# Optimization experiments

Hardware: AMD Instinct MI355X
Metric: run time of the kernel (lower is better)

The kernel has to match this reference:

```python
import jax, jax.numpy as jnp
import numpy as np
import math

DN = ('NCHW', 'OIHW', 'NCHW')

def conv2d(x, w, b=None, pad=0):
    y = jax.lax.conv_general_dilated(x, w, (1, 1), [(pad, pad), (pad, pad)], dimension_numbers=DN)
    if b is not None:
        y = y + b[None, :, None, None]
    return y

def group_norm(x, weight, bias, groups=32, eps=1e-5):
    B, C, H, W = x.shape
    xg = x.reshape(B, groups, C // groups, H, W)
    mean = xg.mean(axis=(2, 3, 4), keepdims=True)
    var = xg.var(axis=(2, 3, 4), keepdims=True)
    xg = (xg - mean) * jax.lax.rsqrt(var + eps)
    return xg.reshape(B, C, H, W) * weight[None, :, None, None] + bias[None, :, None, None]

def swish(x):
    return x * jax.nn.sigmoid(x)

def setup_inputs() -> dict:
    key = jax.random.key(0)
    ks = jax.random.split(key, 20)
    B, C, H, W = 8, 192, 48, 48
    emb = 192
    n_div = 12
    Cq = C // n_div  # 16
    s = 0.02
    return {
        'x': jax.random.normal(ks[0], (B, C, H, W), jnp.float32),
        'xe': jax.random.normal(ks[1], (B, C, H, W), jnp.float32),
        'time_emb': jax.random.normal(ks[2], (B, emb), jnp.float32),
        'gn1_w': jnp.ones((C,), jnp.float32),
        'gn1_b': jnp.zeros((C,), jnp.float32),
        'conv1_w': jax.random.normal(ks[3], (C, C, 3, 3), jnp.float32) * s,
        'conv1_b': jnp.zeros((C,), jnp.float32),
        'aff_w': jax.random.normal(ks[4], (2 * C, emb), jnp.float32) * s,
        'aff_b': jnp.zeros((2 * C,), jnp.float32),
        'gn2_w': jnp.ones((C,), jnp.float32),
        'gn2_b': jnp.zeros((C,), jnp.float32),
        'conv2_w': jax.random.normal(ks[5], (C, C, 3, 3), jnp.float32) * s,
        'conv2_b': jnp.zeros((C,), jnp.float32),
        'q_w': jax.random.normal(ks[6], (Cq, C, 1, 1), jnp.float32) * s,
        'kv_w': jax.random.normal(ks[7], (2 * Cq, C, 1, 1), jnp.float32) * s,
        'out_w': jax.random.normal(ks[8], (C, Cq, 3, 3), jnp.float32) * s,
        'out_b': jnp.zeros((C,), jnp.float32),
    }

def reference(x, xe, time_emb, gn1_w, gn1_b, conv1_w, conv1_b, aff_w, aff_b,
              gn2_w, gn2_b, conv2_w, conv2_b, q_w, kv_w, out_w, out_b):
    B, C, H, W = x.shape
    n_head, n_div = 1, 12
    head_dim = C // (n_head * n_div)

    # ----- ResnetBlock -----
    h = conv2d(swish(group_norm(x, gn1_w, gn1_b)), conv1_w, conv1_b, pad=1)
    # FeatureWiseAffine (use_affine_level=True)
    gb = time_emb @ aff_w.T + aff_b          # [B, 2C]
    gamma, beta = jnp.split(gb, 2, axis=1)   # each [B, C]
    gb_sum = 0.5 * (gamma + beta)[:, :, None, None]
    h = h + gb_sum * h + gb_sum
    h = conv2d(swish(group_norm(h, gn2_w, gn2_b)), conv2_w, conv2_b, pad=1)
    xres = h + x  # res_conv is Identity (dim == dim_out)

    # ----- CrossAttention -----
    Ye, Xe = xe.shape[-2], xe.shape[-1]
    query = conv2d(xres, q_w).reshape(B, n_head, head_dim, H, W)
    kv = conv2d(xe, kv_w).reshape(B, n_head, head_dim * 2, Ye, Xe)
    key_, value = jnp.split(kv, 2, axis=2)
    scale = 1.0 / math.sqrt(C // n_div)
    attn = jnp.einsum('bnchw,bncyx->bnhwyx', query, key_) * scale
    attn = jax.nn.softmax(attn.reshape(B, n_head, H, W, -1), axis=-1)
    attn = attn.reshape(B, n_head, H, W, Ye, Xe)
    out = jnp.einsum('bnhwyx,bncyx->bnchw', attn, value)
    out = conv2d(out.reshape(B, C // n_div, H, W), out_w, out_b, pad=1)
    return out + xres
```

## Files before the change

kernel.cpp:

```cpp
#include <hip/hip_runtime.h>
#include <hip/hip_bf16.h>

#define NB 8
#define NC 192
#define NH 48
#define NW 48
#define NP 2304
#define NGROUPS 32
#define CPG 6
#define NEMB 192
#define NCQ 16

#define PH 50
#define PWS 52
#define ACT_T_ELEMS ((size_t)NB * PH * PWS * NC)
#define AOT_ELEMS   ((size_t)NB * PH * PWS * 16)

typedef __attribute__((ext_vector_type(4))) short s16x4;
typedef __attribute__((ext_vector_type(8))) short s16x8;
typedef __attribute__((ext_vector_type(4))) float f32x4;

static __device__ inline short f2bf(float v) {
  __hip_bfloat16 h = __float2bfloat16(v);
  return *(short*)&h;
}

__global__ __launch_bounds__(256) void megaprep_kernel(
    const float* __restrict__ conv1w, const float* __restrict__ conv2w,
    const float* __restrict__ outw, const float* __restrict__ qw,
    const float* __restrict__ kvw, const float* __restrict__ emb,
    const float* __restrict__ affw, const float* __restrict__ affb,
    short* __restrict__ wbuf1, short* __restrict__ wbuf2, short* __restrict__ wbufo,
    short* __restrict__ awq, short* __restrict__ awkv,
    float* __restrict__ gbsum, short* __restrict__ actt, short* __restrict__ aot) {
  int bx = blockIdx.x;
  int tid = threadIdx.x;
  const float SC = 0.36067376022224085f;
  if (bx < 2592) {
    const float* w = (bx < 1296) ? conv1w : conv2w;
    short* wb      = (bx < 1296) ? wbuf1 : wbuf2;
    int i = ((bx < 1296) ? bx : bx - 1296) * 256 + tid;
    int j  = i & 7;
    int l  = (i >> 3) & 63;
    int cf = (i >> 9) % 12;
    int tk = (i >> 9) / 12;
    int t  = tk % 9;
    int kc = tk / 9;
    int co = cf * 16 + (l & 15);
    int ci = kc * 32 + (l >> 4) * 8 + j;
    wb[i] = f2bf(w[((size_t)co * NC + ci) * 9 + t]);
  } else if (bx < 2808) {
    int i = (bx - 2592) * 256 + tid;
    int j  = i & 7;
    int l  = (i >> 3) & 63;
    int cf = (i >> 9) % 12;
    int t  = (i >> 9) / 12;
    int co = cf * 16 + (l & 15);
    int ci = (l >> 4) * 8 + j;
    wbufo[i] = (ci < 16) ? f2bf(outw[((size_t)co * 16 + ci) * 9 + t]) : (short)0;
  } else if (bx < 2820) {
    int i = (bx - 2808) * 256 + tid;
    int j = i & 7, l = (i >> 3) & 63, rest = i >> 9;
    int kc = rest;
    int co = (l & 15);
    int ci = kc * 32 + (l >> 4) * 8 + j;
    awq[i] = f2bf(qw[(size_t)co * NC + ci] * SC);
  } else if (bx < 2844) {
    int i = (bx - 2820) * 256 + tid;
    int j = i & 7, l = (i >> 3) & 63, rest = i >> 9;
    int m = rest % 2, kc = rest / 2;
    int co = m * 16 + (l & 15);
    int ci = kc * 32 + (l >> 4) * 8 + j;
    awkv[i] = f2bf(kvw[(size_t)co * NC + ci]);
  } else if (bx < 2850) {
    int i = (bx - 2844) * 256 + tid;
    if (i < NB * NC) {
      int b = i / NC;
      int c = i - b * NC;
      const float* e  = emb + b * NEMB;
      const float* w0 = affw + c * NEMB;
      const float* w1 = affw + (c + NC) * NEMB;
      float s = 0.f;
      for (int j = 0; j < NEMB; ++j) s += e[j] * (w0[j] + w1[j]);
      gbsum[i] = 0.5f * (s + affb[c] + affb[c + NC]);
    }
  } else if (bx < 3154) {
    int rel = bx - 2850;
    int b = rel / 38, xb = rel - b * 38;
    int i = xb * 256 + tid;
    if (i < 9600) {
      int c4 = i % 48;
      int r  = i / 48;
      size_t off;
      if (r < 52)       off = ((size_t)0 * PWS + r) * NC;
      else if (r < 104) off = ((size_t)49 * PWS + (r - 52)) * NC;
      else if (r < 152) off = ((size_t)(r - 104 + 1) * PWS + 0) * NC;
      else              off = ((size_t)(r - 152 + 1) * PWS + 49) * NC;
      *(s16x4*)(&actt[(size_t)b * PH * PWS * NC + off + c4 * 4]) = (s16x4){0, 0, 0, 0};
    }
  } else {
    int b = bx - 3154;
    for (int i = tid; i < 784; i += 256) {
      int c4  = i & 3;
      int pos = i >> 2;
      int r, col;
      if (pos < 50)       { r = 0;  col = pos; }
      else if (pos < 100) { r = 49; col = pos - 50; }
      else if (pos < 148) { r = pos - 100 + 1; col = 0; }
      else                { r = pos - 148 + 1; col = 49; }
      *(s16x4*)(&aot[(((size_t)b * PH + r) * PWS + col) * 16 + c4 * 4]) = (s16x4){0, 0, 0, 0};
    }
  }
}

__global__ __launch_bounds__(192) void gn_stats_part_kernel(const float* __restrict__ in,
                                                            float* __restrict__ part) {
  int bg = blockIdx.x, seg = blockIdx.y;
  const float4* p = (const float4*)(in + (size_t)bg * (CPG * NP) + seg * 2304);
  float s = 0.f, s2 = 0.f;
  for (int i = threadIdx.x; i < 576; i += 192) {
    float4 v = p[i];
    s  += v.x + v.y + v.z + v.w;
    s2 += v.x * v.x + v.y * v.y + v.z * v.z + v.w * v.w;
  }
#pragma unroll
  for (int off = 32; off > 0; off >>= 1) {
    s  += __shfl_down(s, off);
    s2 += __shfl_down(s2, off);
  }
  __shared__ float red[6];
  int wave = threadIdx.x >> 6;
  if ((threadIdx.x & 63) == 0) { red[wave * 2] = s; red[wave * 2 + 1] = s2; }
  __syncthreads();
  if (threadIdx.x == 0) {
    part[(bg * 6 + seg) * 2]     = red[0] + red[2] + red[4];
    part[(bg * 6 + seg) * 2 + 1] = red[1] + red[3] + red[5];
  }
}

__global__ __launch_bounds__(256) void gn_apply_t_kernel(const float* __restrict__ in,
                                                         const float* __restrict__ gnpart,
                                                         const float* __restrict__ gw,
                                                         const float* __restrict__ gb,
                                                         short* __restrict__ actt) {
  __shared__ float tile[48 * 193];
  __shared__ float sst[32][2];
  int bh = blockIdx.x;
  int b = bh / NH;
  int h = bh - b * NH;
  int tid = threadIdx.x;
  if (tid < 32) {
    float S = 0.f, S2 = 0.f;
#pragma unroll
    for (int k = 0; k < 6; ++k) {
      S  += gnpart[((b * 32 + tid) * 6 + k) * 2];
      S2 += gnpart[((b * 32 + tid) * 6 + k) * 2 + 1];
    }
    const float invN = 1.f / (float)(CPG * NP);
    float mean = S * invN;
    float var  = S2 * invN - mean * mean;
    sst[tid][0] = mean;
    sst[tid][1] = rsqrtf(var + 1e-5f);
  }
  __syncthreads();
  for (int i = tid; i < 2304; i += 256) {
    int c = i / 12;
    int w = (i % 12) * 4;
    float4 v = *(const float4*)(in + (((size_t)b * NC + c) * NH + h) * NW + w);
    float sc = sst[c / CPG][1] * gw[c];
    float sh = gb[c] - sst[c / CPG][0] * sc;
    float y;
    y = v.x * sc + sh; tile[(w + 0) * 193 + c] = y / (1.f + __expf(-y));
    y = v.y * sc + sh; tile[(w + 1) * 193 + c] = y / (1.f + __expf(-y));
    y = v.z * sc + sh; tile[(w + 2) * 193 + c] = y / (1.f + __expf(-y));
    y = v.w * sc + sh; tile[(w + 3) * 193 + c] = y / (1.f + __expf(-y));
  }
  __syncthreads();
  short* dst = actt + (((size_t)b * PH + h + 1) * PWS + 1) * NC;
  for (int i = tid; i < 2304; i += 256) {
    int w  = i / 48;
    int c4 = (i - w * 48) * 4;
    s16x4 o;
    o.x = f2bf(tile[w * 193 + c4 + 0]);
    o.y = f2bf(tile[w * 193 + c4 + 1]);
    o.z = f2bf(tile[w * 193 + c4 + 2]);
    o.w = f2bf(tile[w * 193 + c4 + 3]);
    *(s16x4*)(dst + (size_t)w * NC + c4) = o;
  }
}

template <int NM, bool ISKV>
__global__ __launch_bounds__(192) void qkv_fused_kernel(const float* __restrict__ X,
                                                        const short* __restrict__ aw,
                                                        short* __restrict__ KQ,
                                                        short* __restrict__ VTb) {
  __shared__ float tile[48 * 193];
  int bh = blockIdx.x;
  int b = bh / NH;
  int h = bh - b * NH;
  int tid = threadIdx.x;
  for (int i = tid; i < 2304; i += 192) {
    int c = i / 12;
    int w = (i % 12) * 4;
    float4 v = *(const float4*)(X + (((size_t)b * NC + c) * NH + h) * NW + w);
    tile[(w + 0) * 193 + c] = v.x;
    tile[(w + 1) * 193 + c] = v.y;
    tile[(w + 2) * 193 + c] = v.z;
    tile[(w + 3) * 193 + c] = v.w;
  }
  __syncthreads();
  int lane = tid & 63, wv = tid >> 6;
  int g = lane >> 4, ql = lane & 15;
  int pxl = wv * 16 + ql;
  int p   = h * NW + pxl;

  f32x4 acc[NM];
#pragma unroll
  for (int m = 0; m < NM; ++m) acc[m] = (f32x4){0.f, 0.f, 0.f, 0.f};

  const float* bp = &tile[pxl * 193 + g * 8];
#pragma unroll
  for (int kc = 0; kc < 6; ++kc) {
    s16x8 bf;
#pragma unroll
    for (int j = 0; j < 8; ++j) bf[j] = f2bf(bp[kc * 32 + j]);
#pragma unroll
    for (int m = 0; m < NM; ++m) {
      s16x8 af = *(const s16x8*)(aw + ((size_t)(kc * NM + m) * 64 + lane) * 8);
      acc[m] = __builtin_amdgcn_mfma_f32_16x16x32_bf16(af, bf, acc[m], 0, 0, 0);
    }
  }
  s16x4 o0;
  o0.x = f2bf(acc[0][0]); o0.y = f2bf(acc[0][1]);
  o0.z = f2bf(acc[0][2]); o0.w = f2bf(acc[0][3]);
  *(s16x4*)(KQ + ((size_t)b * NP + p) * 32 + g * 4) = o0;
  *(s16x4*)(KQ + ((size_t)b * NP + p) * 32 + 16 + g * 4) = (s16x4){0, 0, 0, 0};
  if (ISKV) {
#pragma unroll
    for (int r = 0; r < 4; ++r)
      VTb[((size_t)b * 16 + g * 4 + r) * NP + p] = f2bf(acc[NM - 1][r]);
  }
}

template <bool AFFINE, bool RESID>
__global__ __launch_bounds__(256) void conv_mfma_kernel(const short* __restrict__ actt,
                                                        const short* __restrict__ wbuf,
                                                        const float* __restrict__ bias,
                                                        const float* __restrict__ gbsum,
                                                        const float* __restrict__ resid,
                                                        float* __restrict__ out) {
  __shared__ short S[2][4][50][40];
  int bs = blockIdx.x;
  int b = bs / 24;
  int strip = bs - b * 24;
  int coB = blockIdx.y;
  int h0 = strip * 2;
  int tid = threadIdx.x;
  int lane = tid & 63, wave = tid >> 6;
  int wy = wave >> 1, wx = wave & 1;
  int g8 = (lane >> 4) * 8;

  f32x4 acc[2][3];
#pragma unroll
  for (int m = 0; m < 2; ++m)
#pragma unroll
    for (int f = 0; f < 3; ++f) acc[m][f] = (f32x4){0.f, 0.f, 0.f, 0.f};

  const size_t actbase = ((size_t)b * PH + h0) * PWS * NC;

  auto stage = [&](int buf, int kc) {
    for (int i = tid; i < 800; i += 256) {
      int ci8 = i & 3;
      int rc  = i >> 2;
      int col = rc % 50, r = rc / 50;
      const s16x8* src = (const s16x8*)(actt + actbase + ((size_t)r * PWS + col) * NC +
                                        kc * 32 + ci8 * 8);
      *(s16x8*)(&S[buf][r][col][ci8 * 8]) = *src;
    }
  };

  stage(0, 0);
  __syncthreads();
  for (int kc = 0; kc < 6; ++kc) {
    if (kc < 5) stage((kc + 1) & 1, kc + 1);
    int cur = kc & 1;
#pragma unroll
    for (int t = 0; t < 9; ++t) {
      int ky = t / 3, kx = t - ky * 3;
      const short* wp = wbuf + ((((size_t)kc * 9 + t) * 12 + (coB * 4 + wy * 2)) * 64 + lane) * 8;
      s16x8 a0 = *(const s16x8*)wp;
      s16x8 a1 = *(const s16x8*)(wp + 64 * 8);
      int row = wx + ky;
#pragma unroll
      for (int f = 0; f < 3; ++f) {
        int col = f * 16 + (lane & 15) + kx;
        s16x8 bf = *(const s16x8*)(&S[cur][row][col][g8]);
        acc[0][f] = __builtin_amdgcn_mfma_f32_16x16x32_bf16(a0, bf, acc[0][f], 0, 0, 0);
        acc[1][f] = __builtin_amdgcn_mfma_f32_16x16x32_bf16(a1, bf, acc[1][f], 0, 0, 0);
      }
    }
    __syncthreads();
  }
  int hout = h0 + wx;
#pragma unroll
  for (int m = 0; m < 2; ++m) {
    int co0 = coB * 64 + wy * 32 + m * 16;
#pragma unroll
    for (int r = 0; r < 4; ++r) {
      int co = co0 + (lane >> 4) * 4 + r;
      float bv = bias[co];
      float s = AFFINE ? gbsum[b * NC + co] : 0.f;
#pragma unroll
      for (int f = 0; f < 3; ++f) {
        int w = f * 16 + (lane & 15);
        size_t o = (((size_t)b * NC + co) * NH + hout) * NW + w;
        float v = acc[m][f][r] + bv;
        if (AFFINE) v = v * (1.f + s) + s;
        if (RESID) v += resid[o];
        out[o] = v;
      }
    }
  }
}

__global__ __launch_bounds__(256) void out_conv_mfma_kernel(const short* __restrict__ aot,
                                                            const short* __restrict__ wbuf,
                                                            const float* __restrict__ bias,
                                                            float* __restrict__ out) {
  __shared__ short S[4][50][40];
  int bs = blockIdx.x;
  int b = bs / 24;
  int strip = bs - b * 24;
  int coB = blockIdx.y;
  int h0 = strip * 2;
  int tid = threadIdx.x;
  int lane = tid & 63, wave = tid >> 6;
  int wy = wave >> 1, wx = wave & 1;
  int g8 = (lane >> 4) * 8;

  f32x4 acc[2][3];
#pragma unroll
  for (int m = 0; m < 2; ++m)
#pragma unroll
    for (int f = 0; f < 3; ++f) acc[m][f] = (f32x4){0.f, 0.f, 0.f, 0.f};

  const size_t base = ((size_t)b * PH + h0) * PWS * 16;
  for (int i = tid; i < 800; i += 256) {
    int ci8 = i & 3;
    int rc  = i >> 2;
    int col = rc % 50, r = rc / 50;
    s16x8 v = (s16x8){0, 0, 0, 0, 0, 0, 0, 0};
    if (ci8 < 2)
      v = *(const s16x8*)(aot + base + ((size_t)r * PWS + col) * 16 + ci8 * 8);
    *(s16x8*)(&S[r][col][ci8 * 8]) = v;
  }
  __syncthreads();
#pragma unroll
  for (int t = 0; t < 9; ++t) {
    int ky = t / 3, kx = t - ky * 3;
    const short* wp = wbuf + (((size_t)t * 12 + (coB * 4 + wy * 2)) * 64 + lane) * 8;
    s16x8 a0 = *(const s16x8*)wp;
    s16x8 a1 = *(const s16x8*)(wp + 64 * 8);
    int row = wx + ky;
#pragma unroll
    for (int f = 0; f < 3; ++f) {
      int col = f * 16 + (lane & 15) + kx;
      s16x8 bf = *(const s16x8*)(&S[row][col][g8]);
      acc[0][f] = __builtin_amdgcn_mfma_f32_16x16x32_bf16(a0, bf, acc[0][f], 0, 0, 0);
      acc[1][f] = __builtin_amdgcn_mfma_f32_16x16x32_bf16(a1, bf, acc[1][f], 0, 0, 0);
    }
  }
  int hout = h0 + wx;
#pragma unroll
  for (int m = 0; m < 2; ++m) {
    int co0 = coB * 64 + wy * 32 + m * 16;
#pragma unroll
    for (int r = 0; r < 4; ++r) {
      int co = co0 + (lane >> 4) * 4 + r;
      float bv = bias[co];
#pragma unroll
      for (int f = 0; f < 3; ++f) {
        int w = f * 16 + (lane & 15);
        size_t o = (((size_t)b * NC + co) * NH + hout) * NW + w;
        out[o] = acc[m][f][r] + bv + out[o];
      }
    }
  }
}

__global__ __launch_bounds__(1024) void attn_mfma_kernel(const short* __restrict__ Qb,
                                                         const short* __restrict__ Kb,
                                                         const short* __restrict__ VTb,
                                                         short* __restrict__ aot) {
  __shared__ float PM[4][4][64], PL[4][4][64];
  __shared__ f32x4 PA[4][4][64];
  int b    = blockIdx.y;
  int tid  = threadIdx.x;
  int lane = tid & 63;
  int w    = tid >> 6;
  int qg   = w & 3, ks = w >> 2;
  int q0   = blockIdx.x * 64 + qg * 16;
  int g    = lane >> 4;
  int ql   = lane & 15;

  s16x8 qfrag = *(const s16x8*)(Qb + ((size_t)b * NP + q0 + ql) * 32 + g * 8);

  int r0 = 8 * (ql >> 2) + (ql & 3);
  const short* Kbase = Kb + (size_t)b * NP * 32 + g * 8;
  const short* Vbase = VTb + ((size_t)b * 16 + ql) * NP;

  f32x4 acc = {0.f, 0.f, 0.f, 0.f};
  float m = -1e30f, l = 0.f;

  int kk = ks * 576;
  s16x8 kf0 = *(const s16x8*)(Kbase + (size_t)(kk + r0) * 32);
  s16x8 kf1 = *(const s16x8*)(Kbase + (size_t)(kk + r0 + 4) * 32);
  s16x8 vf  = *(const s16x8*)(Vbase + kk + g * 8);

  for (int step = 0; step < 18; ++step) {
    int kn = (step < 17) ? kk + 32 : ks * 576;
    s16x8 nk0 = *(const s16x8*)(Kbase + (size_t)(kn + r0) * 32);
    s16x8 nk1 = *(const s16x8*)(Kbase + (size_t)(kn + r0 + 4) * 32);
    s16x8 nv  = *(const s16x8*)(Vbase + kn + g * 8);

    f32x4 z = {0.f, 0.f, 0.f, 0.f};
    f32x4 s0 = __builtin_amdgcn_mfma_f32_16x16x32_bf16(kf0, qfrag, z, 0, 0, 0);
    f32x4 s1 = __builtin_amdgcn_mfma_f32_16x16x32_bf16(kf1, qfrag, z, 0, 0, 0);

    float tm = fmaxf(fmaxf(fmaxf(s0[0], s0[1]), fmaxf(s0[2], s0[3])),
                     fmaxf(fmaxf(s1[0], s1[1]), fmaxf(s1[2], s1[3])));
    if (!__all(tm <= m + 8.0f)) {
      tm = fmaxf(tm, __shfl_xor(tm, 16, 64));
      tm = fmaxf(tm, __shfl_xor(tm, 32, 64));
      float mn = fmaxf(m, tm);
      float corr = exp2f(m - mn);
      m = mn;
      l *= corr;
      acc[0] *= corr; acc[1] *= corr; acc[2] *= corr; acc[3] *= corr;
    }
    float p0 = exp2f(s0[0] - m), p1 = exp2f(s0[1] - m);
    float p2 = exp2f(s0[2] - m), p3 = exp2f(s0[3] - m);
    float p4 = exp2f(s1[0] - m), p5 = exp2f(s1[1] - m);
    float p6 = exp2f(s1[2] - m), p7 = exp2f(s1[3] - m);
    l += ((p0 + p1) + (p2 + p3)) + ((p4 + p5) + (p6 + p7));

    s16x8 pf;
    pf[0] = f2bf(p0); pf[1] = f2bf(p1); pf[2] = f2bf(p2); pf[3] = f2bf(p3);
    pf[4] = f2bf(p4); pf[5] = f2bf(p5); pf[6] = f2bf(p6); pf[7] = f2bf(p7);
    acc = __builtin_amdgcn_mfma_f32_16x16x32_bf16(vf, pf, acc, 0, 0, 0);

    kf0 = nk0; kf1 = nk1; vf = nv; kk = kn;
  }
  PM[ks][qg][lane] = m;
  PL[ks][qg][lane] = l;
  PA[ks][qg][lane] = acc;
  __syncthreads();
  if (ks == 0) {
    float M = PM[0][qg][lane];
#pragma unroll
    for (int k = 1; k < 4; ++k) M = fmaxf(M, PM[k][qg][lane]);
    float L = 0.f;
    f32x4 o = {0.f, 0.f, 0.f, 0.f};
#pragma unroll
    for (int k = 0; k < 4; ++k) {
      float c = exp2f(PM[k][qg][lane] - M);
      L += PL[k][qg][lane] * c;
      f32x4 a = PA[k][qg][lane];
      o[0] += a[0] * c; o[1] += a[1] * c; o[2] += a[2] * c; o[3] += a[3] * c;
    }
    L += __shfl_xor(L, 16, 64);
    L += __shfl_xor(L, 32, 64);
    float inv = 1.f / L;
    int q = q0 + ql;
    int h = q / NW, wcol = q - h * NW;
    s16x4 ov;
    ov.x = f2bf(o[0] * inv);
    ov.y = f2bf(o[1] * inv);
    ov.z = f2bf(o[2] * inv);
    ov.w = f2bf(o[3] * inv);
    *(s16x4*)(aot + (((size_t)b * PH + h + 1) * PWS + wcol + 1) * 16 + g * 4) = ov;
  }
}

extern "C" void kernel_launch(void* const* d_in, const int* in_sizes, int n_in,
                              void* d_out, int out_size, void* d_ws, size_t ws_size,
                              hipStream_t stream) {
  const float* x      = (const float*)d_in[0];
  const float* xe     = (const float*)d_in[1];
  const float* temb   = (const float*)d_in[2];
  const float* gn1w   = (const float*)d_in[3];
  const float* gn1b   = (const float*)d_in[4];
  const float* conv1w = (const float*)d_in[5];
  const float* conv1b = (const float*)d_in[6];
  const float* affw   = (const float*)d_in[7];
  const float* affb   = (const float*)d_in[8];
  const float* gn2w   = (const float*)d_in[9];
  const float* gn2b   = (const float*)d_in[10];
  const float* conv2w = (const float*)d_in[11];
  const float* conv2b = (const float*)d_in[12];
  const float* qw     = (const float*)d_in[13];
  const float* kvw    = (const float*)d_in[14];
  const float* outw   = (const float*)d_in[15];
  const float* outb   = (const float*)d_in[16];
  float* out = (float*)d_out;
  float* ws  = (float*)d_ws;

  float* gbsum  = ws;
  float* gnpart = gbsum + NB * NC;
  short* wbuf1  = (short*)(gnpart + 3072);
  short* wbuf2  = wbuf1 + (size_t)6 * 9 * 12 * 64 * 8;
  short* wbufo  = wbuf2 + (size_t)6 * 9 * 12 * 64 * 8;
  short* awq    = wbufo + (size_t)9 * 12 * 64 * 8;
  short* awkv   = awq + 3072;
  short* actt   = awkv + 6144;
  short* Qb     = actt + ACT_T_ELEMS;
  short* Kb     = Qb + (size_t)NB * NP * 32;
  short* VTb    = Kb + (size_t)NB * NP * 32;
  short* aot    = VTb + (size_t)NB * 16 * NP;

  megaprep_kernel<<<3162, 256, 0, stream>>>(conv1w, conv2w, outw, qw, kvw, temb,
                                            affw, affb, wbuf1, wbuf2, wbufo, awq, awkv,
                                            gbsum, actt, aot);
  qkv_fused_kernel<2, true><<<NB * NH, 192, 0, stream>>>(xe, awkv, Kb, VTb);

  gn_stats_part_kernel<<<dim3(NB * NGROUPS, 6), 192, 0, stream>>>(x, gnpart);
  gn_apply_t_kernel<<<NB * NH, 256, 0, stream>>>(x, gnpart, gn1w, gn1b, actt);
  conv_mfma_kernel<true, false><<<dim3(NB * 24, 3), 256, 0, stream>>>(
      actt, wbuf1, conv1b, gbsum, nullptr, out);
  gn_stats_part_kernel<<<dim3(NB * NGROUPS, 6), 192, 0, stream>>>(out, gnpart);
  gn_apply_t_kernel<<<NB * NH, 256, 0, stream>>>(out, gnpart, gn2w, gn2b, actt);
  conv_mfma_kernel<false, true><<<dim3(NB * 24, 3), 256, 0, stream>>>(
      actt, wbuf2, conv2b, nullptr, x, out);

  qkv_fused_kernel<1, false><<<NB * NH, 192, 0, stream>>>(out, awq, Qb, nullptr);
  attn_mfma_kernel<<<dim3(36, NB), 1024, 0, stream>>>(Qb, Kb, VTb, aot);
  out_conv_mfma_kernel<<<dim3(NB * 24, 3), 256, 0, stream>>>(aot, wbufo, outb, out);
}
```

Baseline: 250.4 us.

## Fuse GN stats into prep and conv epilogue, merge QKV into neighboring kernels

```diff
diff --git a/kernel.cpp b/kernel.cpp
--- a/kernel.cpp
+++ b/kernel.cpp
@@ -25,14 +25,17 @@
   return *(short*)&h;
 }
 
-__global__ __launch_bounds__(256) void megaprep_kernel(
+__global__ __launch_bounds__(256) void front_kernel(
     const float* __restrict__ conv1w, const float* __restrict__ conv2w,
     const float* __restrict__ outw, const float* __restrict__ qw,
     const float* __restrict__ kvw, const float* __restrict__ emb,
     const float* __restrict__ affw, const float* __restrict__ affb,
+    const float* __restrict__ x,
     short* __restrict__ wbuf1, short* __restrict__ wbuf2, short* __restrict__ wbufo,
     short* __restrict__ awq, short* __restrict__ awkv,
-    float* __restrict__ gbsum, short* __restrict__ actt, short* __restrict__ aot) {
+    float* __restrict__ gbsum, short* __restrict__ actt, short* __restrict__ aot,
+    float* __restrict__ gnpartA, float* __restrict__ gnpartB) {
+  __shared__ float red[8];
   int bx = blockIdx.x;
   int tid = threadIdx.x;
   const float SC = 0.36067376022224085f;
@@ -60,8 +63,7 @@
     wbufo[i] = (ci < 16) ? f2bf(outw[((size_t)co * 16 + ci) * 9 + t]) : (short)0;
   } else if (bx < 2820) {
     int i = (bx - 2808) * 256 + tid;
-    int j = i & 7, l = (i >> 3) & 63, rest = i >> 9;
-    int kc = rest;
+    int j = i & 7, l = (i >> 3) & 63, kc = i >> 9;
     int co = (l & 15);
     int ci = kc * 32 + (l >> 4) * 8 + j;
     awq[i] = f2bf(qw[(size_t)co * NC + ci] * SC);
@@ -98,7 +100,7 @@
       else              off = ((size_t)(r - 152 + 1) * PWS + 49) * NC;
       *(s16x4*)(&actt[(size_t)b * PH * PWS * NC + off + c4 * 4]) = (s16x4){0, 0, 0, 0};
     }
-  } else {
+  } else if (bx < 3162) {
     int b = bx - 3154;
     for (int i = tid; i < 784; i += 256) {
       int c4  = i & 3;
@@ -110,39 +112,131 @@
       else                { r = pos - 148 + 1; col = 49; }
       *(s16x4*)(&aot[(((size_t)b * PH + r) * PWS + col) * 16 + c4 * 4]) = (s16x4){0, 0, 0, 0};
     }
-  }
-}
-
-__global__ __launch_bounds__(192) void gn_stats_part_kernel(const float* __restrict__ in,
-                                                            float* __restrict__ part) {
-  int bg = blockIdx.x, seg = blockIdx.y;
-  const float4* p = (const float4*)(in + (size_t)bg * (CPG * NP) + seg * 2304);
-  float s = 0.f, s2 = 0.f;
-  for (int i = threadIdx.x; i < 576; i += 192) {
-    float4 v = p[i];
-    s  += v.x + v.y + v.z + v.w;
-    s2 += v.x * v.x + v.y * v.y + v.z * v.z + v.w * v.w;
-  }
-#pragma unroll
-  for (int off = 32; off > 0; off >>= 1) {
-    s  += __shfl_down(s, off);
-    s2 += __shfl_down(s2, off);
-  }
-  __shared__ float red[6];
-  int wave = threadIdx.x >> 6;
-  if ((threadIdx.x & 63) == 0) { red[wave * 2] = s; red[wave * 2 + 1] = s2; }
-  __syncthreads();
-  if (threadIdx.x == 0) {
-    part[(bg * 6 + seg) * 2]     = red[0] + red[2] + red[4];
-    part[(bg * 6 + seg) * 2 + 1] = red[1] + red[3] + red[5];
-  }
-}
-
-__global__ __launch_bounds__(256) void gn_apply_t_kernel(const float* __restrict__ in,
-                                                         const float* __restrict__ gnpart,
-                                                         const float* __restrict__ gw,
-                                                         const float* __restrict__ gb,
-                                                         short* __restrict__ actt) {
+  } else if (bx < 4698) {
+    int rel = bx - 3162;
+    int bg = rel / 6, seg = rel - bg * 6;
+    const float4* p = (const float4*)(x + (size_t)bg * (CPG * NP) + seg * 2304);
+    float s = 0.f, s2 = 0.f;
+    for (int i = tid; i < 576; i += 256) {
+      float4 v = p[i];
+      s  += v.x + v.y + v.z + v.w;
+      s2 += v.x * v.x + v.y * v.y + v.z * v.z + v.w * v.w;
+    }
+#pragma unroll
+    for (int off = 32; off > 0; off >>= 1) {
+      s  += __shfl_down(s, off);
+      s2 += __shfl_down(s2, off);
+    }
+    int wave = tid >> 6;
+    if ((tid & 63) == 0) { red[wave * 2] = s; red[wave * 2 + 1] = s2; }
+    __syncthreads();
+    if (tid == 0) {
+      gnpartA[(bg * 6 + seg) * 2]     = red[0] + red[2] + red[4] + red[6];
+      gnpartA[(bg * 6 + seg) * 2 + 1] = red[1] + red[3] + red[5] + red[7];
+    }
+  } else {
+    gnpartB[tid] = 0.f;
+    gnpartB[tid + 256] = 0.f;
+  }
+}
+
+__global__ __launch_bounds__(256) void mid1_kernel(
+    const float* __restrict__ xe, const short* __restrict__ awkv,
+    short* __restrict__ Kb, short* __restrict__ VTb,
+    const float* __restrict__ x, const float* __restrict__ gnpartA,
+    const float* __restrict__ gw, const float* __restrict__ gb,
+    short* __restrict__ actt) {
+  __shared__ float tile[48 * 193];
+  __shared__ float sst[32][2];
+  int bx = blockIdx.x;
+  int tid = threadIdx.x;
+  if (bx < 384) {
+    int b = bx / NH, h = bx - (bx / NH) * NH;
+    for (int i = tid; i < 2304; i += 256) {
+      int c = i / 12;
+      int w = (i % 12) * 4;
+      float4 v = *(const float4*)(xe + (((size_t)b * NC + c) * NH + h) * NW + w);
+      tile[(w + 0) * 193 + c] = v.x;
+      tile[(w + 1) * 193 + c] = v.y;
+      tile[(w + 2) * 193 + c] = v.z;
+      tile[(w + 3) * 193 + c] = v.w;
+    }
+    __syncthreads();
+    int lane = tid & 63, wv = tid >> 6;
+    if (wv < 3) {
+      int g = lane >> 4, ql = lane & 15;
+      int pxl = wv * 16 + ql;
+      int p = h * NW + pxl;
+      f32x4 acc0 = {0.f, 0.f, 0.f, 0.f}, acc1 = {0.f, 0.f, 0.f, 0.f};
+      const float* bp = &tile[pxl * 193 + g * 8];
+#pragma unroll
+      for (int kc = 0; kc < 6; ++kc) {
+        s16x8 bf;
+#pragma unroll
+        for (int j = 0; j < 8; ++j) bf[j] = f2bf(bp[kc * 32 + j]);
+        s16x8 a0 = *(const s16x8*)(awkv + ((size_t)(kc * 2 + 0) * 64 + lane) * 8);
+        s16x8 a1 = *(const s16x8*)(awkv + ((size_t)(kc * 2 + 1) * 64 + lane) * 8);
+        acc0 = __builtin_amdgcn_mfma_f32_16x16x32_bf16(a0, bf, acc0, 0, 0, 0);
+        acc1 = __builtin_amdgcn_mfma_f32_16x16x32_bf16(a1, bf, acc1, 0, 0, 0);
+      }
+      s16x4 o0;
+      o0.x = f2bf(acc0[0]); o0.y = f2bf(acc0[1]);
+      o0.z = f2bf(acc0[2]); o0.w = f2bf(acc0[3]);
+      *(s16x4*)(Kb + ((size_t)b * NP + p) * 32 + g * 4) = o0;
+      *(s16x4*)(Kb + ((size_t)b * NP + p) * 32 + 16 + g * 4) = (s16x4){0, 0, 0, 0};
+#pragma unroll
+      for (int r = 0; r < 4; ++r)
+        VTb[((size_t)b * 16 + g * 4 + r) * NP + p] = f2bf(acc1[r]);
+    }
+  } else {
+    int bh = bx - 384;
+    int b = bh / NH, h = bh - (bh / NH) * NH;
+    if (tid < 32) {
+      float S = 0.f, S2 = 0.f;
+#pragma unroll
+      for (int k = 0; k < 6; ++k) {
+        S  += gnpartA[((b * 32 + tid) * 6 + k) * 2];
+        S2 += gnpartA[((b * 32 + tid) * 6 + k) * 2 + 1];
+      }
+      const float invN = 1.f / (float)(CPG * NP);
+      float mean = S * invN;
+      float var  = S2 * invN - mean * mean;
+      sst[tid][0] = mean;
+      sst[tid][1] = rsqrtf(var + 1e-5f);
+    }
+    __syncthreads();
+    for (int i = tid; i < 2304; i += 256) {
+      int c = i / 12;
+      int w = (i % 12) * 4;
+      float4 v = *(const float4*)(x + (((size_t)b * NC + c) * NH + h) * NW + w);
+      float sc = sst[c / CPG][1] * gw[c];
+      float sh = gb[c] - sst[c / CPG][0] * sc;
+      float y;
+      y = v.x * sc + sh; tile[(w + 0) * 193 + c] = y / (1.f + __expf(-y));
+      y = v.y * sc + sh; tile[(w + 1) * 193 + c] = y / (1.f + __expf(-y));
+      y = v.z * sc + sh; tile[(w + 2) * 193 + c] = y / (1.f + __expf(-y));
+      y = v.w * sc + sh; tile[(w + 3) * 193 + c] = y / (1.f + __expf(-y));
+    }
+    __syncthreads();
+    short* dst = actt + (((size_t)b * PH + h + 1) * PWS + 1) * NC;
+    for (int i = tid; i < 2304; i += 256) {
+      int w  = i / 48;
+      int c4 = (i - w * 48) * 4;
+      s16x4 o;
+      o.x = f2bf(tile[w * 193 + c4 + 0]);
+      o.y = f2bf(tile[w * 193 + c4 + 1]);
+      o.z = f2bf(tile[w * 193 + c4 + 2]);
+      o.w = f2bf(tile[w * 193 + c4 + 3]);
+      *(s16x4*)(dst + (size_t)w * NC + c4) = o;
+    }
+  }
+}
+
+__global__ __launch_bounds__(256) void gn_apply_raw_kernel(const float* __restrict__ in,
+                                                           const float* __restrict__ gnpartB,
+                                                           const float* __restrict__ gw,
+                                                           const float* __restrict__ gb,
+                                                           short* __restrict__ actt) {
   __shared__ float tile[48 * 193];
   __shared__ float sst[32][2];
   int bh = blockIdx.x;
@@ -150,12 +244,8 @@
   int h = bh - b * NH;
   int tid = threadIdx.x;
   if (tid < 32) {
-    float S = 0.f, S2 = 0.f;
-#pragma unroll
-    for (int k = 0; k < 6; ++k) {
-      S  += gnpart[((b * 32 + tid) * 6 + k) * 2];
-      S2 += gnpart[((b * 32 + tid) * 6 + k) * 2 + 1];
-    }
+    float S  = gnpartB[(b * 32 + tid) * 2];
+    float S2 = gnpartB[(b * 32 + tid) * 2 + 1];
     const float invN = 1.f / (float)(CPG * NP);
     float mean = S * invN;
     float var  = S2 * invN - mean * mean;
@@ -189,67 +279,16 @@
   }
 }
 
-template <int NM, bool ISKV>
-__global__ __launch_bounds__(192) void qkv_fused_kernel(const float* __restrict__ X,
-                                                        const short* __restrict__ aw,
-                                                        short* __restrict__ KQ,
-                                                        short* __restrict__ VTb) {
-  __shared__ float tile[48 * 193];
-  int bh = blockIdx.x;
-  int b = bh / NH;
-  int h = bh - b * NH;
-  int tid = threadIdx.x;
-  for (int i = tid; i < 2304; i += 192) {
-    int c = i / 12;
-    int w = (i % 12) * 4;
-    float4 v = *(const float4*)(X + (((size_t)b * NC + c) * NH + h) * NW + w);
-    tile[(w + 0) * 193 + c] = v.x;
-    tile[(w + 1) * 193 + c] = v.y;
-    tile[(w + 2) * 193 + c] = v.z;
-    tile[(w + 3) * 193 + c] = v.w;
-  }
-  __syncthreads();
-  int lane = tid & 63, wv = tid >> 6;
-  int g = lane >> 4, ql = lane & 15;
-  int pxl = wv * 16 + ql;
-  int p   = h * NW + pxl;
-
-  f32x4 acc[NM];
-#pragma unroll
-  for (int m = 0; m < NM; ++m) acc[m] = (f32x4){0.f, 0.f, 0.f, 0.f};
-
-  const float* bp = &tile[pxl * 193 + g * 8];
-#pragma unroll
-  for (int kc = 0; kc < 6; ++kc) {
-    s16x8 bf;
-#pragma unroll
-    for (int j = 0; j < 8; ++j) bf[j] = f2bf(bp[kc * 32 + j]);
-#pragma unroll
-    for (int m = 0; m < NM; ++m) {
-      s16x8 af = *(const s16x8*)(aw + ((size_t)(kc * NM + m) * 64 + lane) * 8);
-      acc[m] = __builtin_amdgcn_mfma_f32_16x16x32_bf16(af, bf, acc[m], 0, 0, 0);
-    }
-  }
-  s16x4 o0;
-  o0.x = f2bf(acc[0][0]); o0.y = f2bf(acc[0][1]);
-  o0.z = f2bf(acc[0][2]); o0.w = f2bf(acc[0][3]);
-  *(s16x4*)(KQ + ((size_t)b * NP + p) * 32 + g * 4) = o0;
-  *(s16x4*)(KQ + ((size_t)b * NP + p) * 32 + 16 + g * 4) = (s16x4){0, 0, 0, 0};
-  if (ISKV) {
-#pragma unroll
-    for (int r = 0; r < 4; ++r)
-      VTb[((size_t)b * 16 + g * 4 + r) * NP + p] = f2bf(acc[NM - 1][r]);
-  }
-}
-
-template <bool AFFINE, bool RESID>
+template <bool AFFINE, bool RESID, bool STATS>
 __global__ __launch_bounds__(256) void conv_mfma_kernel(const short* __restrict__ actt,
                                                         const short* __restrict__ wbuf,
                                                         const float* __restrict__ bias,
                                                         const float* __restrict__ gbsum,
                                                         const float* __restrict__ resid,
-                                                        float* __restrict__ out) {
+                                                        float* __restrict__ out,
+                                                        float* __restrict__ gnpartB) {
   __shared__ short S[2][4][50][40];
+  __shared__ float csum[64][2];
   int bs = blockIdx.x;
   int b = bs / 24;
   int strip = bs - b * 24;
@@ -260,6 +299,8 @@
   int wy = wave >> 1, wx = wave & 1;
   int g8 = (lane >> 4) * 8;
 
+  if (STATS && tid < 64) { csum[tid][0] = 0.f; csum[tid][1] = 0.f; }
+
   f32x4 acc[2][3];
 #pragma unroll
   for (int m = 0; m < 2; ++m)
@@ -310,6 +351,7 @@
       int co = co0 + (lane >> 4) * 4 + r;
       float bv = bias[co];
       float s = AFFINE ? gbsum[b * NC + co] : 0.f;
+      float ls = 0.f, ls2 = 0.f;
 #pragma unroll
       for (int f = 0; f < 3; ++f) {
         int w = f * 16 + (lane & 15);
@@ -318,7 +360,29 @@
         if (AFFINE) v = v * (1.f + s) + s;
         if (RESID) v += resid[o];
         out[o] = v;
+        if (STATS) { ls += v; ls2 += v * v; }
       }
+      if (STATS) {
+#pragma unroll
+        for (int off = 1; off < 16; off <<= 1) {
+          ls  += __shfl_xor(ls, off, 64);
+          ls2 += __shfl_xor(ls2, off, 64);
+        }
+        if ((lane & 15) == 0) {
+          int lc = wy * 32 + m * 16 + (lane >> 4) * 4 + r;
+          atomicAdd(&csum[lc][0], ls);
+          atomicAdd(&csum[lc][1], ls2);
+        }
+      }
+    }
+  }
+  if (STATS) {
+    __syncthreads();
+    if (tid < 64) {
+      int co = coB * 64 + tid;
+      int g = co / CPG;
+      atomicAdd(&gnpartB[(b * NGROUPS + g) * 2], csum[tid][0]);
+      atomicAdd(&gnpartB[(b * NGROUPS + g) * 2 + 1], csum[tid][1]);
     }
   }
 }
@@ -388,22 +452,50 @@
   }
 }
 
-__global__ __launch_bounds__(1024) void attn_mfma_kernel(const short* __restrict__ Qb,
+__global__ __launch_bounds__(1024) void attn_mfma_kernel(const float* __restrict__ xres,
+                                                         const short* __restrict__ awq,
                                                          const short* __restrict__ Kb,
                                                          const short* __restrict__ VTb,
                                                          short* __restrict__ aot) {
-  __shared__ float PM[4][4][64], PL[4][4][64];
-  __shared__ f32x4 PA[4][4][64];
+  __shared__ float tile[64 * 193];
+  __shared__ short QL[16][16][32];
+  float (*PM)[4][64] = (float(*)[4][64])tile;
+  float (*PL)[4][64] = (float(*)[4][64])(tile + 1024);
+  f32x4 (*PA)[4][64] = (f32x4(*)[4][64])(tile + 2048);
+
   int b    = blockIdx.y;
   int tid  = threadIdx.x;
   int lane = tid & 63;
   int w    = tid >> 6;
   int qg   = w & 3, ks = w >> 2;
-  int q0   = blockIdx.x * 64 + qg * 16;
+  int p0   = blockIdx.x * 64;
+  int q0   = p0 + qg * 16;
   int g    = lane >> 4;
   int ql   = lane & 15;
 
-  s16x8 qfrag = *(const s16x8*)(Qb + ((size_t)b * NP + q0 + ql) * 32 + g * 8);
+  for (int i = tid; i < 12288; i += 1024) {
+    int c = i >> 6, pl = i & 63;
+    tile[pl * 193 + c] = xres[((size_t)b * NC + c) * NP + p0 + pl];
+  }
+  __syncthreads();
+  {
+    f32x4 qa = {0.f, 0.f, 0.f, 0.f};
+    const float* bp = &tile[(qg * 16 + ql) * 193 + g * 8];
+#pragma unroll
+    for (int kc = 0; kc < 6; ++kc) {
+      s16x8 bf;
+#pragma unroll
+      for (int j = 0; j < 8; ++j) bf[j] = f2bf(bp[kc * 32 + j]);
+      s16x8 af = *(const s16x8*)(awq + ((size_t)(kc * 64 + lane)) * 8);
+      qa = __builtin_amdgcn_mfma_f32_16x16x32_bf16(af, bf, qa, 0, 0, 0);
+    }
+    s16x4 qv;
+    qv.x = f2bf(qa[0]); qv.y = f2bf(qa[1]); qv.z = f2bf(qa[2]); qv.w = f2bf(qa[3]);
+    *(s16x4*)&QL[w][ql][g * 4] = qv;
+    *(s16x4*)&QL[w][ql][16 + g * 4] = (s16x4){0, 0, 0, 0};
+  }
+  __syncthreads();
+  s16x8 qfrag = *(const s16x8*)&QL[w][ql][g * 8];
 
   int r0 = 8 * (ql >> 2) + (ql & 3);
   const short* Kbase = Kb + (size_t)b * NP * 32 + g * 8;
@@ -438,15 +530,15 @@
       l *= corr;
       acc[0] *= corr; acc[1] *= corr; acc[2] *= corr; acc[3] *= corr;
     }
-    float p0 = exp2f(s0[0] - m), p1 = exp2f(s0[1] - m);
-    float p2 = exp2f(s0[2] - m), p3 = exp2f(s0[3] - m);
-    float p4 = exp2f(s1[0] - m), p5 = exp2f(s1[1] - m);
-    float p6 = exp2f(s1[2] - m), p7 = exp2f(s1[3] - m);
-    l += ((p0 + p1) + (p2 + p3)) + ((p4 + p5) + (p6 + p7));
+    float p0e = exp2f(s0[0] - m), p1e = exp2f(s0[1] - m);
+    float p2e = exp2f(s0[2] - m), p3e = exp2f(s0[3] - m);
+    float p4e = exp2f(s1[0] - m), p5e = exp2f(s1[1] - m);
+    float p6e = exp2f(s1[2] - m), p7e = exp2f(s1[3] - m);
+    l += ((p0e + p1e) + (p2e + p3e)) + ((p4e + p5e) + (p6e + p7e));
 
     s16x8 pf;
-    pf[0] = f2bf(p0); pf[1] = f2bf(p1); pf[2] = f2bf(p2); pf[3] = f2bf(p3);
-    pf[4] = f2bf(p4); pf[5] = f2bf(p5); pf[6] = f2bf(p6); pf[7] = f2bf(p7);
+    pf[0] = f2bf(p0e); pf[1] = f2bf(p1e); pf[2] = f2bf(p2e); pf[3] = f2bf(p3e);
+    pf[4] = f2bf(p4e); pf[5] = f2bf(p5e); pf[6] = f2bf(p6e); pf[7] = f2bf(p7e);
     acc = __builtin_amdgcn_mfma_f32_16x16x32_bf16(vf, pf, acc, 0, 0, 0);
 
     kf0 = nk0; kf1 = nk1; vf = nv; kk = kn;
@@ -505,34 +597,28 @@
   float* out = (float*)d_out;
   float* ws  = (float*)d_ws;
 
-  float* gbsum  = ws;
-  float* gnpart = gbsum + NB * NC;
-  short* wbuf1  = (short*)(gnpart + 3072);
-  short* wbuf2  = wbuf1 + (size_t)6 * 9 * 12 * 64 * 8;
-  short* wbufo  = wbuf2 + (size_t)6 * 9 * 12 * 64 * 8;
-  short* awq    = wbufo + (size_t)9 * 12 * 64 * 8;
-  short* awkv   = awq + 3072;
-  short* actt   = awkv + 6144;
-  short* Qb     = actt + ACT_T_ELEMS;
-  short* Kb     = Qb + (size_t)NB * NP * 32;
-  short* VTb    = Kb + (size_t)NB * NP * 32;
-  short* aot    = VTb + (size_t)NB * 16 * NP;
-
-  megaprep_kernel<<<3162, 256, 0, stream>>>(conv1w, conv2w, outw, qw, kvw, temb,
-                                            affw, affb, wbuf1, wbuf2, wbufo, awq, awkv,
-                                            gbsum, actt, aot);
-  qkv_fused_kernel<2, true><<<NB * NH, 192, 0, stream>>>(xe, awkv, Kb, VTb);
-
-  gn_stats_part_kernel<<<dim3(NB * NGROUPS, 6), 192, 0, stream>>>(x, gnpart);
-  gn_apply_t_kernel<<<NB * NH, 256, 0, stream>>>(x, gnpart, gn1w, gn1b, actt);
-  conv_mfma_kernel<true, false><<<dim3(NB * 24, 3), 256, 0, stream>>>(
-      actt, wbuf1, conv1b, gbsum, nullptr, out);
-  gn_stats_part_kernel<<<dim3(NB * NGROUPS, 6), 192, 0, stream>>>(out, gnpart);
-  gn_apply_t_kernel<<<NB * NH, 256, 0, stream>>>(out, gnpart, gn2w, gn2b, actt);
-  conv_mfma_kernel<false, true><<<dim3(NB * 24, 3), 256, 0, stream>>>(
-      actt, wbuf2, conv2b, nullptr, x, out);
-
-  qkv_fused_kernel<1, false><<<NB * NH, 192, 0, stream>>>(out, awq, Qb, nullptr);
-  attn_mfma_kernel<<<dim3(36, NB), 1024, 0, stream>>>(Qb, Kb, VTb, aot);
+  float* gbsum   = ws;
+  float* gnpartA = gbsum + NB * NC;
+  float* gnpartB = gnpartA + 3072;
+  short* wbuf1   = (short*)(gnpartB + 512);
+  short* wbuf2   = wbuf1 + (size_t)6 * 9 * 12 * 64 * 8;
+  short* wbufo   = wbuf2 + (size_t)6 * 9 * 12 * 64 * 8;
+  short* awq     = wbufo + (size_t)9 * 12 * 64 * 8;
+  short* awkv    = awq + 3072;
+  short* actt    = awkv + 6144;
+  short* Kb      = actt + ACT_T_ELEMS;
+  short* VTb     = Kb + (size_t)NB * NP * 32;
+  short* aot     = VTb + (size_t)NB * 16 * NP;
+
+  front_kernel<<<4699, 256, 0, stream>>>(conv1w, conv2w, outw, qw, kvw, temb,
+                                         affw, affb, x, wbuf1, wbuf2, wbufo, awq, awkv,
+                                         gbsum, actt, aot, gnpartA, gnpartB);
+  mid1_kernel<<<768, 256, 0, stream>>>(xe, awkv, Kb, VTb, x, gnpartA, gn1w, gn1b, actt);
+  conv_mfma_kernel<true, false, true><<<dim3(NB * 24, 3), 256, 0, stream>>>(
+      actt, wbuf1, conv1b, gbsum, nullptr, out, gnpartB);
+  gn_apply_raw_kernel<<<NB * NH, 256, 0, stream>>>(out, gnpartB, gn2w, gn2b, actt);
+  conv_mfma_kernel<false, true, false><<<dim3(NB * 24, 3), 256, 0, stream>>>(
+      actt, wbuf2, conv2b, nullptr, x, out, nullptr);
+  attn_mfma_kernel<<<dim3(36, NB), 1024, 0, stream>>>(out, awq, Kb, VTb, aot);
   out_conv_mfma_kernel<<<dim3(NB * 24, 3), 256, 0, stream>>>(aot, wbufo, outb, out);
 }
```

New measurement: 280.8 us. 1.12x slower.
